# Kernel optimization log

Hardware: AMD Instinct MI355X
Metric: run time of the kernel (lower is better)

Reference implementation:

```python
import jax, jax.numpy as jnp
import numpy as np

MARGIN_RANK = 0.1
MARGIN_OCC = 0.3
LAMBDA_OCC = 1.5
MIN_PIXELS = 20


def setup_inputs() -> dict:
    key = jax.random.key(0)
    k1, k2, k3, k4, k5, k6 = jax.random.split(key, 6)
    B, N, R, H, W = 4, 32, 64, 480, 640
    return {
        "depth_pred": jax.random.uniform(k1, (B, 1, H, W), dtype=jnp.float32),
        "masks": jax.random.uniform(k2, (B, N, H, W), dtype=jnp.float32),
        "subj_idx": jax.random.randint(k3, (B, R), 0, N, dtype=jnp.int32),
        "obj_idx": jax.random.randint(k4, (B, R), 0, N, dtype=jnp.int32),
        "rel_type": jax.random.randint(k5, (B, R), 0, 3, dtype=jnp.int32),  # 0=front,1=behind,2=occludes
        "confidence": jax.random.uniform(k6, (B, R), dtype=jnp.float32),
    }


def reference(depth_pred, masks, subj_idx, obj_idx, rel_type, confidence):
    depth = depth_pred[:, 0]                       # (B, H, W)
    dt = depth.dtype
    m = (masks > 0.5).astype(dt)                   # binarize masks, (B, N, H, W)
    cnt = jnp.sum(m, axis=(-2, -1))                # (B, N) pixels per object
    # per-object mean depth over masked region (single fused segment-reduce)
    d_obj = jnp.einsum("bnhw,bhw->bn", m, depth) / jnp.maximum(cnt, 1.0)
    valid_obj = cnt >= MIN_PIXELS                  # (B, N)

    # 'behind' relations are rewritten as swapped 'front'
    is_behind = rel_type == 1
    sA = jnp.where(is_behind, obj_idx, subj_idx)   # (B, R)
    sB = jnp.where(is_behind, subj_idx, obj_idx)

    take = lambda a, idx: jnp.take_along_axis(a, idx, axis=1)
    dA, dB = take(d_obj, sA), take(d_obj, sB)
    valid = take(valid_obj, sA) & take(valid_obj, sB)  # (B, R)

    is_occ = rel_type == 2
    margin = jnp.where(is_occ, jnp.asarray(MARGIN_OCC, dt), jnp.asarray(MARGIN_RANK, dt))
    coeff = jnp.where(is_occ, jnp.asarray(LAMBDA_OCC, dt), jnp.asarray(1.0, dt))

    violation = jax.nn.relu(dA - dB + margin)
    w = coeff * confidence * valid.astype(dt)
    total = jnp.sum(w * violation)
    count = jnp.sum(valid).astype(dt)
    return jnp.where(count > 0, total / jnp.maximum(count, 1.0), jnp.asarray(0.0, dt))
```

## Files before the change

### kernel.cpp

```cpp
#include <hip/hip_runtime.h>

#define BDIM 4
#define NOBJ 32
#define HH 480
#define WW 640
#define RREL 64
#define HW (HH * WW)
#define HW4 (HW / 4)
#define CH 16
#define CHUNK4 (HW4 / CH)
#define BN (BDIM * NOBJ)
#define BR (BDIM * RREL)

__global__ __launch_bounds__(256) void rdl_mask_stats(
    const float* __restrict__ depth, const float* __restrict__ masks,
    float* __restrict__ sumd, unsigned int* __restrict__ cnt)
{
    const int blk = blockIdx.x;
    const int c   = blk & (CH - 1);
    const int bn  = blk / CH;
    const int b   = bn / NOBJ;

    const float4* __restrict__ mp =
        (const float4*)masks + (size_t)bn * HW4 + (size_t)c * CHUNK4;
    const float4* __restrict__ dp =
        (const float4*)depth + (size_t)b * HW4 + (size_t)c * CHUNK4;

    float s = 0.0f;
    unsigned int k = 0;
    for (int i = threadIdx.x; i < CHUNK4; i += 256) {
        const float4 m = mp[i];
        const float4 d = dp[i];
        if (m.x > 0.5f) { s += d.x; ++k; }
        if (m.y > 0.5f) { s += d.y; ++k; }
        if (m.z > 0.5f) { s += d.z; ++k; }
        if (m.w > 0.5f) { s += d.w; ++k; }
    }

    for (int off = 32; off > 0; off >>= 1) {
        s += __shfl_down(s, off, 64);
        k += __shfl_down(k, off, 64);
    }
    __shared__ float        ls[4];
    __shared__ unsigned int lk[4];
    const int lane = threadIdx.x & 63;
    const int wave = threadIdx.x >> 6;
    if (lane == 0) { ls[wave] = s; lk[wave] = k; }
    __syncthreads();
    if (threadIdx.x == 0) {
        const float        st = ls[0] + ls[1] + ls[2] + ls[3];
        const unsigned int kt = lk[0] + lk[1] + lk[2] + lk[3];
        atomicAdd(&sumd[bn], st);
        atomicAdd(&cnt[bn], kt);
    }
}

__global__ __launch_bounds__(256) void rdl_loss(
    const float* __restrict__ sumd, const unsigned int* __restrict__ cnt,
    const int* __restrict__ subj, const int* __restrict__ obj,
    const int* __restrict__ rel, const float* __restrict__ conf,
    float* __restrict__ out)
{
    __shared__ float dobj[BN];
    __shared__ int   vobj[BN];
    const int t = threadIdx.x;
    if (t < BN) {
        const unsigned int c = cnt[t];
        dobj[t] = sumd[t] / fmaxf((float)c, 1.0f);
        vobj[t] = (c >= 20u) ? 1 : 0;
    }
    __syncthreads();

    float total;
    int   count;
    {
        const int b  = t / RREL;
        const int rt = rel[t];
        const int si = subj[t];
        const int oi = obj[t];
        const int ia = (rt == 1) ? oi : si;
        const int ib = (rt == 1) ? si : oi;
        const float dA = dobj[b * NOBJ + ia];
        const float dB = dobj[b * NOBJ + ib];
        const int   v  = vobj[b * NOBJ + ia] & vobj[b * NOBJ + ib];
        const float margin = (rt == 2) ? 0.3f : 0.1f;
        const float coeff  = (rt == 2) ? 1.5f : 1.0f;
        const float viol   = fmaxf(dA - dB + margin, 0.0f);
        total = coeff * conf[t] * (float)v * viol;
        count = v;
    }
    for (int off = 32; off > 0; off >>= 1) {
        total += __shfl_down(total, off, 64);
        count += __shfl_down(count, off, 64);
    }
    __shared__ float ts[4];
    __shared__ int   cs[4];
    const int lane = t & 63;
    const int wave = t >> 6;
    if (lane == 0) { ts[wave] = total; cs[wave] = count; }
    __syncthreads();
    if (t == 0) {
        const float tt = ts[0] + ts[1] + ts[2] + ts[3];
        const int   cc = cs[0] + cs[1] + cs[2] + cs[3];
        out[0] = (cc > 0) ? tt / fmaxf((float)cc, 1.0f) : 0.0f;
    }
}

extern "C" void kernel_launch(void* const* d_in, const int* in_sizes, int n_in,
                              void* d_out, int out_size, void* d_ws, size_t ws_size,
                              hipStream_t stream)
{
    const float* depth = (const float*)d_in[0];
    const float* masks = (const float*)d_in[1];
    const int*   subj  = (const int*)d_in[2];
    const int*   obj   = (const int*)d_in[3];
    const int*   rel   = (const int*)d_in[4];
    const float* conf  = (const float*)d_in[5];
    float*       out   = (float*)d_out;

    float*        sumd = (float*)d_ws;
    unsigned int* cnt  = (unsigned int*)((char*)d_ws + BN * sizeof(float));

    hipMemsetAsync(d_ws, 0, BN * (sizeof(float) + sizeof(unsigned int)), stream);

    rdl_mask_stats<<<BN * CH, 256, 0, stream>>>(depth, masks, sumd, cnt);
    rdl_loss<<<1, 256, 0, stream>>>(sumd, cnt, subj, obj, rel, conf, out);
}
```

Baseline: 240.7 us.

## Replace atomics and memset with per-block partials, reorder blocks, nontemporal mask loads

Each block now writes its partial sum and count to its own slot, and the loss kernel reduces the 16 chunk partials per object. This removes the memset launch and the global atomics. The block index is remapped so that consecutive blocks handle different objects of the same chunk, which can raise L2 reuse of the shared depth data. Mask loads are marked nontemporal so the streamed masks are less likely to evict depth from cache. Counts are accumulated in float, which stays exact at these sizes.

```diff
diff --git a/kernel.cpp b/kernel.cpp
--- a/kernel.cpp
+++ b/kernel.cpp
@@ -2,61 +2,59 @@
 
 #define BDIM 4
 #define NOBJ 32
-#define HH 480
-#define WW 640
 #define RREL 64
-#define HW (HH * WW)
+#define HW 307200
 #define HW4 (HW / 4)
 #define CH 16
 #define CHUNK4 (HW4 / CH)
 #define BN (BDIM * NOBJ)
+#define NBLK (BN * CH)
 #define BR (BDIM * RREL)
+
+typedef float vfloat4 __attribute__((ext_vector_type(4)));
 
 __global__ __launch_bounds__(256) void rdl_mask_stats(
     const float* __restrict__ depth, const float* __restrict__ masks,
-    float* __restrict__ sumd, unsigned int* __restrict__ cnt)
+    float2* __restrict__ part)
 {
     const int blk = blockIdx.x;
-    const int c   = blk & (CH - 1);
-    const int bn  = blk / CH;
-    const int b   = bn / NOBJ;
+    const int c   = blk >> 7;
+    const int bn  = blk & (BN - 1);
+    const int b   = bn >> 5;
 
-    const float4* __restrict__ mp =
-        (const float4*)masks + (size_t)bn * HW4 + (size_t)c * CHUNK4;
-    const float4* __restrict__ dp =
-        (const float4*)depth + (size_t)b * HW4 + (size_t)c * CHUNK4;
+    const vfloat4* __restrict__ mp =
+        (const vfloat4*)masks + (size_t)bn * HW4 + (size_t)c * CHUNK4;
+    const vfloat4* __restrict__ dp =
+        (const vfloat4*)depth + (size_t)b * HW4 + (size_t)c * CHUNK4;
 
     float s = 0.0f;
-    unsigned int k = 0;
+    float k = 0.0f;
     for (int i = threadIdx.x; i < CHUNK4; i += 256) {
-        const float4 m = mp[i];
-        const float4 d = dp[i];
-        if (m.x > 0.5f) { s += d.x; ++k; }
-        if (m.y > 0.5f) { s += d.y; ++k; }
-        if (m.z > 0.5f) { s += d.z; ++k; }
-        if (m.w > 0.5f) { s += d.w; ++k; }
+        const vfloat4 m = __builtin_nontemporal_load(&mp[i]);
+        const vfloat4 d = dp[i];
+        if (m.x > 0.5f) { s += d.x; k += 1.0f; }
+        if (m.y > 0.5f) { s += d.y; k += 1.0f; }
+        if (m.z > 0.5f) { s += d.z; k += 1.0f; }
+        if (m.w > 0.5f) { s += d.w; k += 1.0f; }
     }
 
     for (int off = 32; off > 0; off >>= 1) {
         s += __shfl_down(s, off, 64);
         k += __shfl_down(k, off, 64);
     }
-    __shared__ float        ls[4];
-    __shared__ unsigned int lk[4];
+    __shared__ float ls[4], lk[4];
     const int lane = threadIdx.x & 63;
     const int wave = threadIdx.x >> 6;
     if (lane == 0) { ls[wave] = s; lk[wave] = k; }
     __syncthreads();
     if (threadIdx.x == 0) {
-        const float        st = ls[0] + ls[1] + ls[2] + ls[3];
-        const unsigned int kt = lk[0] + lk[1] + lk[2] + lk[3];
-        atomicAdd(&sumd[bn], st);
-        atomicAdd(&cnt[bn], kt);
+        part[blk] = make_float2(ls[0] + ls[1] + ls[2] + ls[3],
+                                lk[0] + lk[1] + lk[2] + lk[3]);
     }
 }
 
 __global__ __launch_bounds__(256) void rdl_loss(
-    const float* __restrict__ sumd, const unsigned int* __restrict__ cnt,
+    const float2* __restrict__ part,
     const int* __restrict__ subj, const int* __restrict__ obj,
     const int* __restrict__ rel, const float* __restrict__ conf,
     float* __restrict__ out)
@@ -65,9 +63,14 @@
     __shared__ int   vobj[BN];
     const int t = threadIdx.x;
     if (t < BN) {
-        const unsigned int c = cnt[t];
-        dobj[t] = sumd[t] / fmaxf((float)c, 1.0f);
-        vobj[t] = (c >= 20u) ? 1 : 0;
+        float s = 0.0f, k = 0.0f;
+        #pragma unroll
+        for (int c = 0; c < CH; ++c) {
+            const float2 p = part[c * BN + t];
+            s += p.x; k += p.y;
+        }
+        dobj[t] = s / fmaxf(k, 1.0f);
+        vobj[t] = (k >= 20.0f) ? 1 : 0;
     }
     __syncthreads();
 
@@ -118,11 +121,8 @@
     const float* conf  = (const float*)d_in[5];
     float*       out   = (float*)d_out;
 
-    float*        sumd = (float*)d_ws;
-    unsigned int* cnt  = (unsigned int*)((char*)d_ws + BN * sizeof(float));
+    float2* part = (float2*)d_ws;
 
-    hipMemsetAsync(d_ws, 0, BN * (sizeof(float) + sizeof(unsigned int)), stream);
-
-    rdl_mask_stats<<<BN * CH, 256, 0, stream>>>(depth, masks, sumd, cnt);
-    rdl_loss<<<1, 256, 0, stream>>>(sumd, cnt, subj, obj, rel, conf, out);
+    rdl_mask_stats<<<NBLK, 256, 0, stream>>>(depth, masks, part);
+    rdl_loss<<<1, 256, 0, stream>>>(part, subj, obj, rel, conf, out);
 }
```

Result: faster. 229.4 us (-4.7%).
